# Performance work log

Hardware: AMD Instinct MI355X
Metric: run time of the kernel (lower is better)

## Reference

```python
import jax, jax.numpy as jnp
import numpy as np

N, D, H = 50000, 128, 2        # nodes, hidden_size(=ffn_size=out_channels), heads
E = 800000                      # edges
C = D                           # per-head out_channels (PyG TransformerConv)
EPS = 1e-5

def layer_norm(x, g, b):
    mu = jnp.mean(x, axis=-1, keepdims=True)
    var = jnp.mean((x - mu) ** 2, axis=-1, keepdims=True)
    return (x - mu) / jnp.sqrt(var + EPS) * g + b

def setup_inputs() -> dict:
    key = jax.random.key(0)
    ks = jax.random.split(key, 16)
    s_in = 1.0 / np.sqrt(D)
    s_ffn = 1.0 / np.sqrt(D)
    return {
        "x": jax.random.normal(ks[0], (N, D), jnp.float32),
        "edge_index": jax.random.randint(ks[1], (2, E), 0, N, jnp.int64),
        "ln1_g": jnp.ones((D,), jnp.float32),
        "ln1_b": jnp.zeros((D,), jnp.float32),
        "Wq": jax.random.normal(ks[2], (D, H * C), jnp.float32) * s_in,
        "bq": jnp.zeros((H * C,), jnp.float32),
        "Wk": jax.random.normal(ks[3], (D, H * C), jnp.float32) * s_in,
        "bk": jnp.zeros((H * C,), jnp.float32),
        "Wv": jax.random.normal(ks[4], (D, H * C), jnp.float32) * s_in,
        "bv": jnp.zeros((H * C,), jnp.float32),
        "Wskip": jax.random.normal(ks[5], (D, C), jnp.float32) * s_in,
        "bskip": jnp.zeros((C,), jnp.float32),
        "ln2_g": jnp.ones((D,), jnp.float32),
        "ln2_b": jnp.zeros((D,), jnp.float32),
        "W1": jax.random.normal(ks[6], (D, D), jnp.float32) * s_ffn,
        "b1": jnp.zeros((D,), jnp.float32),
        "W2": jax.random.normal(ks[7], (D, D), jnp.float32) * s_ffn,
        "b2": jnp.zeros((D,), jnp.float32),
    }

def reference(x, edge_index, ln1_g, ln1_b, Wq, bq, Wk, bk, Wv, bv,
              Wskip, bskip, ln2_g, ln2_b, W1, b1, W2, b2):
    src, dst = edge_index[0], edge_index[1]  # messages flow src(j) -> dst(i)
    n = x.shape[0]

    # --- self-attention block (pre-norm) ---
    y = layer_norm(x, ln1_g, ln1_b)
    q = (y @ Wq + bq).reshape(n, H, C)
    k = (y @ Wk + bk).reshape(n, H, C)
    v = (y @ Wv + bv).reshape(n, H, C)

    # per-edge attention logits [E, H]
    alpha = jnp.einsum('ehc,ehc->eh', q[dst], k[src]) / jnp.sqrt(jnp.float32(C))
    # softmax over incoming edges of each dst node
    m = jax.ops.segment_max(alpha, dst, num_segments=n)          # [N, H]
    p = jnp.exp(alpha - m[dst])                                  # [E, H]
    denom = jax.ops.segment_sum(p, dst, num_segments=n)          # [N, H]
    a = p / denom[dst]                                           # [E, H]

    attn = jax.ops.segment_sum(a[:, :, None] * v[src], dst, num_segments=n)  # [N,H,C]
    out = attn.mean(axis=1) + (y @ Wskip + bskip)  # concat=False mean + root skip
    x = x + out  # residual (dropout is identity at eval)

    # --- FFN block (pre-norm) ---
    h = layer_norm(x, ln2_g, ln2_b)
    h = jax.nn.gelu(h @ W1 + b1, approximate=False) @ W2 + b2
    return x + h
```

## Files before the change

kernel.cpp:

```cpp
#include <hip/hip_runtime.h>
#include <hip/hip_bf16.h>
#include <math.h>


typedef unsigned short u16;
using short8 = __attribute__((ext_vector_type(8))) short;
using f32x4  = __attribute__((ext_vector_type(4))) float;
using f32x2  = __attribute__((ext_vector_type(2))) float;

__device__ __forceinline__ float bf2f(u16 u) {
    return __uint_as_float(((unsigned int)u) << 16);
}
__device__ __forceinline__ u16 f2bf(float f) {
    __hip_bfloat16 h = __float2bfloat16(f);
    return __builtin_bit_cast(u16, h);
}
__device__ __forceinline__ float bfe(short8 v, int j) {
    return bf2f((u16)v[j]);
}
__device__ __forceinline__ void fp8x4_to_f32(int w, float* out) {
    f32x2 lo = __builtin_amdgcn_cvt_pk_f32_fp8(w, false);
    f32x2 hi = __builtin_amdgcn_cvt_pk_f32_fp8(w, true);
    out[0] = lo[0]; out[1] = lo[1]; out[2] = hi[0]; out[3] = hi[1];
}
__device__ __forceinline__ unsigned pack_fp8x4(float4 f) {
    unsigned w = 0;
    w = (unsigned)__builtin_amdgcn_cvt_pk_fp8_f32(f.x, f.y, (int)w, false);
    w = (unsigned)__builtin_amdgcn_cvt_pk_fp8_f32(f.z, f.w, (int)w, true);
    return w;
}

__global__ __launch_bounds__(256) void fused_prep_ln(
    const float* __restrict__ x, const float* __restrict__ ln1g,
    const float* __restrict__ ln1b,
    const float* __restrict__ Wq, const float* __restrict__ Wk,
    const float* __restrict__ Wv, const float* __restrict__ Ws,
    const float* __restrict__ W1, const float* __restrict__ W2,
    const float* __restrict__ bq, const float* __restrict__ bk,
    const float* __restrict__ bv, const float* __restrict__ bs,
    u16* __restrict__ wt, float* __restrict__ bc,
    u16* __restrict__ y, int* __restrict__ cnt, int n,
    const int* __restrict__ edst, int e, int histBlocks)
{
    if (blockIdx.x < (unsigned)histBlocks) {
        int stride = histBlocks * 256;
        for (int i = blockIdx.x * 256 + threadIdx.x; i < e; i += stride)
            atomicAdd(&cnt[edst[i]], 1);
        return;
    }
    int gsz = (gridDim.x - histBlocks) * 256;
    int gtid = (blockIdx.x - histBlocks) * 256 + threadIdx.x;

    for (int i = gtid; i < 147456 + 896; i += gsz) {
        if (i < 147456) {
            const float* W; int N; int base;
            if      (i <  32768) { W = Wq; N = 256; base = 0; }
            else if (i <  65536) { W = Wk; N = 256; base = 32768; }
            else if (i <  98304) { W = Wv; N = 256; base = 65536; }
            else if (i < 114688) { W = Ws; N = 128; base = 98304; }
            else if (i < 131072) { W = W1; N = 128; base = 114688; }
            else                 { W = W2; N = 128; base = 131072; }
            int j = i - base;
            int nIdx = j >> 7, k = j & 127;
            wt[i] = f2bf(W[(size_t)k * N + nIdx]);
        } else {
            int j = i - 147456;
            float v;
            if      (j < 256) v = bq[j];
            else if (j < 512) v = bk[j - 256];
            else if (j < 768) v = bv[j - 512];
            else              v = bs[j - 768];
            bc[j] = v;
        }
    }
    int lane = threadIdx.x & 63;
    int gw = gtid >> 6, nw = gsz >> 6;
    for (int row = gw; row < n; row += nw) {
        size_t base = (size_t)row * 128;
        float v0 = x[base + lane];
        float v1 = x[base + 64 + lane];
        float s1 = v0 + v1, s2 = v0 * v0 + v1 * v1;
        for (int o = 1; o <= 32; o <<= 1) {
            s1 += __shfl_xor(s1, o);
            s2 += __shfl_xor(s2, o);
        }
        float mu = s1 * (1.f / 128.f);
        float var = s2 * (1.f / 128.f) - mu * mu;
        float rstd = rsqrtf(var + 1e-5f);
        y[base + lane]      = f2bf((v0 - mu) * rstd * ln1g[lane] + ln1b[lane]);
        y[base + 64 + lane] = f2bf((v1 - mu) * rstd * ln1g[64 + lane] + ln1b[64 + lane]);
    }
}

__global__ __launch_bounds__(256) void scan_block_sum(const int* __restrict__ cnt,
                                                      int* __restrict__ bsum, int n) {
    __shared__ int s[256];
    int idx = blockIdx.x * 256 + threadIdx.x;
    s[threadIdx.x] = (idx < n) ? cnt[idx] : 0;
    __syncthreads();
    for (int o = 128; o > 0; o >>= 1) {
        if (threadIdx.x < o) s[threadIdx.x] += s[threadIdx.x + o];
        __syncthreads();
    }
    if (threadIdx.x == 0) bsum[blockIdx.x] = s[0];
}
__global__ __launch_bounds__(256) void scan_partials(const int* __restrict__ bsum,
                                                     int* __restrict__ bsumex, int nb) {
    __shared__ int s[256];
    int t = threadIdx.x;
    int v = (t < nb) ? bsum[t] : 0;
    s[t] = v;
    __syncthreads();
    for (int o = 1; o < 256; o <<= 1) {
        int add = (t >= o) ? s[t - o] : 0;
        __syncthreads();
        s[t] += add;
        __syncthreads();
    }
    bsumex[t] = s[t] - v;
}
__global__ __launch_bounds__(256) void scan_write(const int* __restrict__ cnt,
                                                  const int* __restrict__ bsumex,
                                                  int* __restrict__ rowptr,
                                                  int* __restrict__ cursor, int n, int etot) {
    __shared__ int s[256];
    int t = threadIdx.x;
    int idx = blockIdx.x * 256 + t;
    int v = (idx < n) ? cnt[idx] : 0;
    s[t] = v;
    __syncthreads();
    for (int o = 1; o < 256; o <<= 1) {
        int add = (t >= o) ? s[t - o] : 0;
        __syncthreads();
        s[t] += add;
        __syncthreads();
    }
    if (idx < n) {
        int ex = bsumex[blockIdx.x] + s[t] - v;
        rowptr[idx] = ex;
        cursor[idx] = ex;
    }
    if (idx == 0) rowptr[n] = etot;
}

__global__ __launch_bounds__(256, 6) void qkv_gemm(
    const u16* __restrict__ A, const u16* __restrict__ Bt,
    const float* __restrict__ bias, u16* __restrict__ qkv,
    float* __restrict__ skip, int n,
    const int* __restrict__ dst, const int* __restrict__ src,
    int* __restrict__ cursor, int* __restrict__ esrc, int e, int scatBlocks)
{
    __shared__ float epi[4][32 * 33];
    if (blockIdx.x < (unsigned)scatBlocks) {
        int stride = scatBlocks * 256;
        int i = blockIdx.x * 256 + threadIdx.x;
        for (; i + 3 * stride < e; i += 4 * stride) {
            int d0 = dst[i],              s0 = src[i];
            int d1 = dst[i + stride],     s1 = src[i + stride];
            int d2 = dst[i + 2 * stride], s2 = src[i + 2 * stride];
            int d3 = dst[i + 3 * stride], s3 = src[i + 3 * stride];
            int p0 = atomicAdd(&cursor[d0], 1);
            int p1 = atomicAdd(&cursor[d1], 1);
            int p2 = atomicAdd(&cursor[d2], 1);
            int p3 = atomicAdd(&cursor[d3], 1);
            esrc[p0] = s0; esrc[p1] = s1; esrc[p2] = s2; esrc[p3] = s3;
        }
        for (; i < e; i += stride) {
            int p = atomicAdd(&cursor[dst[i]], 1);
            esrc[p] = src[i];
        }
        return;
    }
    int bid = blockIdx.x - scatBlocks;
    int wc = threadIdx.x >> 6, lane = threadIdx.x & 63;
    int r0 = bid * 32;
    int lm = lane & 15, quad = lane >> 4;

    int ar0 = r0 + lm;       if (ar0 > n - 1) ar0 = n - 1;
    int ar1 = r0 + 16 + lm;  if (ar1 > n - 1) ar1 = n - 1;
    const u16* aB0 = A + (size_t)ar0 * 128 + quad * 8;
    const u16* aB1 = A + (size_t)ar1 * 128 + quad * 8;
    short8 a0_0 = *(const short8*)(aB0 + 0);
    short8 a0_1 = *(const short8*)(aB0 + 32);
    short8 a0_2 = *(const short8*)(aB0 + 64);
    short8 a0_3 = *(const short8*)(aB0 + 96);
    short8 a1_0 = *(const short8*)(aB1 + 0);
    short8 a1_1 = *(const short8*)(aB1 + 32);
    short8 a1_2 = *(const short8*)(aB1 + 64);
    short8 a1_3 = *(const short8*)(aB1 + 96);
    asm volatile("" : "+v"(a0_0), "+v"(a0_1), "+v"(a0_2), "+v"(a0_3),
                      "+v"(a1_0), "+v"(a1_1), "+v"(a1_2), "+v"(a1_3));

    int rr = lane & 31, hh = lane >> 5;
    int row = r0 + rr;
    bool rowOk = row < n;
    float* ep = epi[wc];

    for (int by = 0; by < 7; ++by) {
        int c0 = by * 128;
        const u16* bBase = Bt + (size_t)(c0 + wc * 32 + lm) * 128 + quad * 8;
        f32x4 acc[2][2] = {};
#pragma unroll
        for (int kx = 0; kx < 4; ++kx) {
            short8 a0 = (kx == 0) ? a0_0 : (kx == 1) ? a0_1 : (kx == 2) ? a0_2 : a0_3;
            short8 a1 = (kx == 0) ? a1_0 : (kx == 1) ? a1_1 : (kx == 2) ? a1_2 : a1_3;
#pragma unroll
            for (int j = 0; j < 2; ++j) {
                short8 bj = *(const short8*)(bBase + (size_t)j * 16 * 128 + kx * 32);
                acc[0][j] = __builtin_amdgcn_mfma_f32_16x16x32_bf16(a0, bj, acc[0][j], 0, 0, 0);
                acc[1][j] = __builtin_amdgcn_mfma_f32_16x16x32_bf16(a1, bj, acc[1][j], 0, 0, 0);
            }
        }
#pragma unroll
        for (int j = 0; j < 2; ++j) {
            float bv = bias[c0 + wc * 32 + j * 16 + lm];
#pragma unroll
            for (int rt = 0; rt < 2; ++rt)
#pragma unroll
                for (int i2 = 0; i2 < 4; ++i2)
                    ep[(rt * 16 + quad * 4 + i2) * 33 + j * 16 + lm]
                        = acc[rt][j][i2] + bv;
        }
        if (rowOk) {
            const float* ws = ep + rr * 33 + hh * 16;
            int colW = wc * 32 + hh * 16;
            if (c0 < 256) {
                u16* dp = qkv + (size_t)row * 640 + c0 + colW;
                short8 o0, o1;
#pragma unroll
                for (int jj = 0; jj < 8; ++jj) {
                    o0[jj] = (short)f2bf(ws[jj]);
                    o1[jj] = (short)f2bf(ws[8 + jj]);
                }
                *(short8*)(dp + 0) = o0;
                *(short8*)(dp + 8) = o1;
            } else if (c0 < 512) {
                unsigned char* kb = (unsigned char*)qkv + (size_t)row * 1280
                                    + 512 + (c0 - 256) + colW;
                uint4 o;
                o.x = pack_fp8x4(make_float4(ws[0],  ws[1],  ws[2],  ws[3]));
                o.y = pack_fp8x4(make_float4(ws[4],  ws[5],  ws[6],  ws[7]));
                o.z = pack_fp8x4(make_float4(ws[8],  ws[9],  ws[10], ws[11]));
                o.w = pack_fp8x4(make_float4(ws[12], ws[13], ws[14], ws[15]));
                *(uint4*)kb = o;
            } else if (c0 < 768) {
                u16* dp = qkv + (size_t)row * 640 + 384 + (c0 - 512) + colW;
                short8 o0, o1;
#pragma unroll
                for (int jj = 0; jj < 8; ++jj) {
                    o0[jj] = (short)f2bf(ws[jj]);
                    o1[jj] = (short)f2bf(ws[8 + jj]);
                }
                *(short8*)(dp + 0) = o0;
                *(short8*)(dp + 8) = o1;
            } else {
                float* dp = skip + (size_t)row * 128 + colW;
#pragma unroll
                for (int m2 = 0; m2 < 4; ++m2)
                    *(float4*)(dp + m2 * 4) = *(const float4*)(ws + m2 * 4);
            }
        }
    }
}

__global__ __launch_bounds__(256) void attn_kernel(
    const u16* __restrict__ qkv, const int* __restrict__ rowptr,
    const int* __restrict__ esrc, const float* __restrict__ x,
    float* __restrict__ sx, const float* __restrict__ g2,
    const float* __restrict__ b2, u16* __restrict__ y, int n)
{
    int wid = threadIdx.x >> 6, lane = threadIdx.x & 63;
    int i = blockIdx.x * 4 + wid;
    if (i >= n) return;
    int slot = lane >> 5;
    int sub  = lane & 15;
    int colOff = ((lane >> 4) & 1) * 128 + sub * 8;

    const float scale = 0.08838834764831845f;
    short8 q8 = *(const short8*)(qkv + (size_t)i * 640 + colOff);
    float qf[8];
#pragma unroll
    for (int j = 0; j < 8; ++j) qf[j] = bfe(q8, j) * scale;

    int beg = rowptr[i], end = rowptr[i + 1];
    float l = 0.f;
    float acc[8] = {};

    int t = beg + slot;
    for (; t + 6 < end; t += 8) {
        int s0 = esrc[t], s1 = esrc[t + 2], s2 = esrc[t + 4], s3 = esrc[t + 6];
        const u16* n0 = qkv + (size_t)s0 * 640;
        const u16* n1 = qkv + (size_t)s1 * 640;
        const u16* n2 = qkv + (size_t)s2 * 640;
        const u16* n3 = qkv + (size_t)s3 * 640;
        uint2 kw0 = *(const uint2*)((const unsigned char*)(n0 + 256) + colOff);
        uint2 kw1 = *(const uint2*)((const unsigned char*)(n1 + 256) + colOff);
        uint2 kw2 = *(const uint2*)((const unsigned char*)(n2 + 256) + colOff);
        uint2 kw3 = *(const uint2*)((const unsigned char*)(n3 + 256) + colOff);
        short8 v0 = *(const short8*)(n0 + 384 + colOff);
        short8 v1 = *(const short8*)(n1 + 384 + colOff);
        short8 v2 = *(const short8*)(n2 + 384 + colOff);
        short8 v3 = *(const short8*)(n3 + 384 + colOff);
        float k0f[8], k1f[8], k2f[8], k3f[8];
        fp8x4_to_f32((int)kw0.x, k0f); fp8x4_to_f32((int)kw0.y, k0f + 4);
        fp8x4_to_f32((int)kw1.x, k1f); fp8x4_to_f32((int)kw1.y, k1f + 4);
        fp8x4_to_f32((int)kw2.x, k2f); fp8x4_to_f32((int)kw2.y, k2f + 4);
        fp8x4_to_f32((int)kw3.x, k3f); fp8x4_to_f32((int)kw3.y, k3f + 4);
        float d0 = 0.f, d1 = 0.f, d2 = 0.f, d3 = 0.f;
#pragma unroll
        for (int j = 0; j < 8; ++j) {
            d0 += qf[j] * k0f[j];
            d1 += qf[j] * k1f[j];
            d2 += qf[j] * k2f[j];
            d3 += qf[j] * k3f[j];
        }
#pragma unroll
        for (int o = 1; o <= 8; o <<= 1) {
            d0 += __shfl_xor(d0, o);
            d1 += __shfl_xor(d1, o);
            d2 += __shfl_xor(d2, o);
            d3 += __shfl_xor(d3, o);
        }
        float w0 = __expf(d0), w1 = __expf(d1);
        float w2 = __expf(d2), w3 = __expf(d3);
        l += w0 + w1 + w2 + w3;
#pragma unroll
        for (int j = 0; j < 8; ++j)
            acc[j] += w0 * bfe(v0, j) + w1 * bfe(v1, j)
                    + w2 * bfe(v2, j) + w3 * bfe(v3, j);
    }
    for (; t < end; t += 2) {
        int s0 = esrc[t];
        const u16* n0 = qkv + (size_t)s0 * 640;
        uint2 kw0 = *(const uint2*)((const unsigned char*)(n0 + 256) + colOff);
        short8 v0 = *(const short8*)(n0 + 384 + colOff);
        float k0f[8];
        fp8x4_to_f32((int)kw0.x, k0f); fp8x4_to_f32((int)kw0.y, k0f + 4);
        float d0 = 0.f;
#pragma unroll
        for (int j = 0; j < 8; ++j) d0 += qf[j] * k0f[j];
#pragma unroll
        for (int o = 1; o <= 8; o <<= 1) d0 += __shfl_xor(d0, o);
        float w0 = __expf(d0);
        l += w0;
#pragma unroll
        for (int j = 0; j < 8; ++j) acc[j] += w0 * bfe(v0, j);
    }

    l += __shfl_xor(l, 32);
    float inv = (l > 0.f) ? (1.f / l) : 0.f;
#pragma unroll
    for (int j = 0; j < 8; ++j) {
        acc[j] = (acc[j] + __shfl_xor(acc[j], 32)) * inv;
        acc[j] = 0.5f * (acc[j] + __shfl_xor(acc[j], 16));
    }

    if (lane < 16) {
        size_t base = (size_t)i * 128 + sub * 8;
        float4 xv0 = *(const float4*)(x + base);
        float4 xv1 = *(const float4*)(x + base + 4);
        float4 sk0 = *(const float4*)(sx + base);
        float4 sk1 = *(const float4*)(sx + base + 4);
        float r[8];
        r[0] = xv0.x + sk0.x + acc[0]; r[1] = xv0.y + sk0.y + acc[1];
        r[2] = xv0.z + sk0.z + acc[2]; r[3] = xv0.w + sk0.w + acc[3];
        r[4] = xv1.x + sk1.x + acc[4]; r[5] = xv1.y + sk1.y + acc[5];
        r[6] = xv1.z + sk1.z + acc[6]; r[7] = xv1.w + sk1.w + acc[7];
        *(float4*)(sx + base)     = make_float4(r[0], r[1], r[2], r[3]);
        *(float4*)(sx + base + 4) = make_float4(r[4], r[5], r[6], r[7]);
        float s1 = 0.f, s2 = 0.f;
#pragma unroll
        for (int j = 0; j < 8; ++j) { s1 += r[j]; s2 += r[j] * r[j]; }
#pragma unroll
        for (int o = 1; o <= 8; o <<= 1) {
            s1 += __shfl_xor(s1, o);
            s2 += __shfl_xor(s2, o);
        }
        float mu = s1 * (1.f / 128.f);
        float var = s2 * (1.f / 128.f) - mu * mu;
        float rstd = rsqrtf(var + 1e-5f);
        short8 o8;
#pragma unroll
        for (int j = 0; j < 8; ++j)
            o8[j] = (short)f2bf((r[j] - mu) * rstd * g2[sub * 8 + j] + b2[sub * 8 + j]);
        *(short8*)(y + base) = o8;
    }
}

__global__ __launch_bounds__(256) void ffn_kernel(
    const u16* __restrict__ y2, const u16* __restrict__ W1T,
    const float* __restrict__ b1, const u16* __restrict__ W2T,
    const float* __restrict__ b2, const float* __restrict__ x2,
    float* __restrict__ out, int n)
{
    __shared__ u16 t1[64 * 136];
    int wid = threadIdx.x >> 6, lane = threadIdx.x & 63;
    int lm = lane & 15, quad = lane >> 4;
    int r0 = blockIdx.x * 64 + wid * 16;

    const u16* aBase = y2 + (size_t)(r0 + lm) * 128 + quad * 8;
    f32x4 acc[8] = {};
#pragma unroll
    for (int kk = 0; kk < 128; kk += 32) {
        short8 a0 = *(const short8*)(aBase + kk);
#pragma unroll
        for (int j = 0; j < 8; ++j) {
            short8 bj = *(const short8*)(W1T + (size_t)(j * 16 + lm) * 128 + quad * 8 + kk);
            acc[j] = __builtin_amdgcn_mfma_f32_16x16x32_bf16(a0, bj, acc[j], 0, 0, 0);
        }
    }
#pragma unroll
    for (int j = 0; j < 8; ++j) {
        int col = j * 16 + lm;
        float bv = b1[col];
#pragma unroll
        for (int i2 = 0; i2 < 4; ++i2) {
            int rl = wid * 16 + quad * 4 + i2;
            float v = acc[j][i2] + bv;
            v = 0.5f * v * (1.f + erff(v * 0.70710678118654752f));
            t1[rl * 136 + col] = f2bf(v);
        }
    }
    __syncthreads();

    f32x4 acc2[8] = {};
#pragma unroll
    for (int kk = 0; kk < 128; kk += 32) {
        short8 a0 = *(const short8*)(t1 + (wid * 16 + lm) * 136 + quad * 8 + kk);
#pragma unroll
        for (int j = 0; j < 8; ++j) {
            short8 bj = *(const short8*)(W2T + (size_t)(j * 16 + lm) * 128 + quad * 8 + kk);
            acc2[j] = __builtin_amdgcn_mfma_f32_16x16x32_bf16(a0, bj, acc2[j], 0, 0, 0);
        }
    }
#pragma unroll
    for (int j = 0; j < 8; ++j) {
        int col = j * 16 + lm;
        float bv = b2[col];
#pragma unroll
        for (int i2 = 0; i2 < 4; ++i2) {
            int row = r0 + quad * 4 + i2;
            if (row >= n) continue;
            size_t ob = (size_t)row * 128 + col;
            out[ob] = acc2[j][i2] + bv + x2[ob];
        }
    }
}

extern "C" void kernel_launch(void* const* d_in, const int* in_sizes, int n_in,
                              void* d_out, int out_size, void* d_ws, size_t ws_size,
                              hipStream_t stream)
{
    const float* x    = (const float*)d_in[0];
    const int*   ei   = (const int*)d_in[1];

    int n = in_sizes[0] / 128;
    int e = in_sizes[1] / 2;
    const int* src  = ei;
    const int* dstp = ei + e;

    char* w = (char*)d_ws;
    size_t off = 0;
    auto alloc = [&](size_t bytes) -> void* {
        void* p = w + off;
        off = (off + bytes + 255) & ~(size_t)255;
        return p;
    };
    u16*   y    = (u16*)alloc((size_t)n * 128 * 2);
    u16*   qkv  = (u16*)alloc((size_t)n * 640 * 2);
    float* sx   = (float*)alloc((size_t)n * 128 * 4);
    u16*   wt   = (u16*)alloc((size_t)147456 * 2);
    float* bc   = (float*)alloc(896 * 4);
    int* cnt    = (int*)alloc((size_t)n * 4);
    int* cursor = (int*)alloc((size_t)n * 4);
    int* rowptr = (int*)alloc(((size_t)n + 1) * 4);
    int* esrc   = (int*)alloc((size_t)e * 4);
    int* bsum   = (int*)alloc(1024);
    int* bsumex = (int*)alloc(1024);

    int gr   = (n + 63) / 64;
    int gr32 = (n + 31) / 32;
    int nb   = (n + 255) / 256;
    int scatBlocks = 512;
    int histBlocks = 512;

    hipMemsetAsync(cnt, 0, (size_t)n * sizeof(int), stream);
    fused_prep_ln<<<2048 + histBlocks, 256, 0, stream>>>(
        x, (const float*)d_in[2], (const float*)d_in[3],
        (const float*)d_in[4], (const float*)d_in[6], (const float*)d_in[8],
        (const float*)d_in[10], (const float*)d_in[14], (const float*)d_in[16],
        (const float*)d_in[5], (const float*)d_in[7], (const float*)d_in[9],
        (const float*)d_in[11], wt, bc, y, cnt, n, dstp, e, histBlocks);
    scan_block_sum<<<nb, 256, 0, stream>>>(cnt, bsum, n);
    scan_partials<<<1, 256, 0, stream>>>(bsum, bsumex, nb);
    scan_write<<<nb, 256, 0, stream>>>(cnt, bsumex, rowptr, cursor, n, e);
    qkv_gemm<<<scatBlocks + gr32, 256, 0, stream>>>(
        y, wt, bc, qkv, sx, n, dstp, src, cursor, esrc, e, scatBlocks);
    attn_kernel<<<(n + 3) / 4, 256, 0, stream>>>(qkv, rowptr, esrc, x, sx,
                                                 (const float*)d_in[12],
                                                 (const float*)d_in[13], y, n);
    ffn_kernel<<<gr, 256, 0, stream>>>(y, wt + 114688, (const float*)d_in[15],
                                       wt + 131072, (const float*)d_in[17],
                                       sx, (float*)d_out, n);
}
```

Measured before the change: 405.2 us.

## Record per-edge rank during histogram to replace scatter atomics in CSR build

The histogram pass now stores the value returned by each atomicAdd as that edge's rank within its destination bucket. The scatter pass then computes each edge's CSR slot as rowptr[dst] + rank with plain loads, so the second round of contended atomics and the cursor array are no longer needed. This costs an extra E-sized int array written and read back, and the number of scatter blocks is doubled. Edge order within each destination changes, which can slightly perturb the floating-point summation order.

```diff
diff --git a/kernel.cpp b/kernel.cpp
--- a/kernel.cpp
+++ b/kernel.cpp
@@ -39,13 +39,13 @@
     const float* __restrict__ bq, const float* __restrict__ bk,
     const float* __restrict__ bv, const float* __restrict__ bs,
     u16* __restrict__ wt, float* __restrict__ bc,
-    u16* __restrict__ y, int* __restrict__ cnt, int n,
+    u16* __restrict__ y, int* __restrict__ cnt, int* __restrict__ rank, int n,
     const int* __restrict__ edst, int e, int histBlocks)
 {
     if (blockIdx.x < (unsigned)histBlocks) {
         int stride = histBlocks * 256;
         for (int i = blockIdx.x * 256 + threadIdx.x; i < e; i += stride)
-            atomicAdd(&cnt[edst[i]], 1);
+            rank[i] = atomicAdd(&cnt[edst[i]], 1);
         return;
     }
     int gsz = (gridDim.x - histBlocks) * 256;
@@ -122,7 +122,7 @@
 __global__ __launch_bounds__(256) void scan_write(const int* __restrict__ cnt,
                                                   const int* __restrict__ bsumex,
                                                   int* __restrict__ rowptr,
-                                                  int* __restrict__ cursor, int n, int etot) {
+                                                  int n, int etot) {
     __shared__ int s[256];
     int t = threadIdx.x;
     int idx = blockIdx.x * 256 + t;
@@ -135,11 +135,7 @@
         s[t] += add;
         __syncthreads();
     }
-    if (idx < n) {
-        int ex = bsumex[blockIdx.x] + s[t] - v;
-        rowptr[idx] = ex;
-        cursor[idx] = ex;
-    }
+    if (idx < n) rowptr[idx] = bsumex[blockIdx.x] + s[t] - v;
     if (idx == 0) rowptr[n] = etot;
 }
 
@@ -148,27 +144,24 @@
     const float* __restrict__ bias, u16* __restrict__ qkv,
     float* __restrict__ skip, int n,
     const int* __restrict__ dst, const int* __restrict__ src,
-    int* __restrict__ cursor, int* __restrict__ esrc, int e, int scatBlocks)
+    const int* __restrict__ rank, const int* __restrict__ rowptr,
+    int* __restrict__ esrc, int e, int scatBlocks)
 {
     __shared__ float epi[4][32 * 33];
     if (blockIdx.x < (unsigned)scatBlocks) {
         int stride = scatBlocks * 256;
         int i = blockIdx.x * 256 + threadIdx.x;
         for (; i + 3 * stride < e; i += 4 * stride) {
-            int d0 = dst[i],              s0 = src[i];
-            int d1 = dst[i + stride],     s1 = src[i + stride];
-            int d2 = dst[i + 2 * stride], s2 = src[i + 2 * stride];
-            int d3 = dst[i + 3 * stride], s3 = src[i + 3 * stride];
-            int p0 = atomicAdd(&cursor[d0], 1);
-            int p1 = atomicAdd(&cursor[d1], 1);
-            int p2 = atomicAdd(&cursor[d2], 1);
-            int p3 = atomicAdd(&cursor[d3], 1);
-            esrc[p0] = s0; esrc[p1] = s1; esrc[p2] = s2; esrc[p3] = s3;
-        }
-        for (; i < e; i += stride) {
-            int p = atomicAdd(&cursor[dst[i]], 1);
-            esrc[p] = src[i];
-        }
+            int i1 = i + stride, i2 = i + 2 * stride, i3 = i + 3 * stride;
+            int d0 = dst[i],  d1 = dst[i1], d2 = dst[i2], d3 = dst[i3];
+            int r0 = rank[i], r1 = rank[i1], r2 = rank[i2], r3 = rank[i3];
+            int s0 = src[i],  s1 = src[i1], s2 = src[i2], s3 = src[i3];
+            int p0 = rowptr[d0], p1 = rowptr[d1], p2 = rowptr[d2], p3 = rowptr[d3];
+            esrc[p0 + r0] = s0; esrc[p1 + r1] = s1;
+            esrc[p2 + r2] = s2; esrc[p3 + r3] = s3;
+        }
+        for (; i < e; i += stride)
+            esrc[rowptr[dst[i]] + rank[i]] = src[i];
         return;
     }
     int bid = blockIdx.x - scatBlocks;
@@ -472,7 +465,7 @@
     u16*   wt   = (u16*)alloc((size_t)147456 * 2);
     float* bc   = (float*)alloc(896 * 4);
     int* cnt    = (int*)alloc((size_t)n * 4);
-    int* cursor = (int*)alloc((size_t)n * 4);
+    int* rankA  = (int*)alloc((size_t)e * 4);
     int* rowptr = (int*)alloc(((size_t)n + 1) * 4);
     int* esrc   = (int*)alloc((size_t)e * 4);
     int* bsum   = (int*)alloc(1024);
@@ -481,7 +474,7 @@
     int gr   = (n + 63) / 64;
     int gr32 = (n + 31) / 32;
     int nb   = (n + 255) / 256;
-    int scatBlocks = 512;
+    int scatBlocks = 1024;
     int histBlocks = 512;
 
     hipMemsetAsync(cnt, 0, (size_t)n * sizeof(int), stream);
@@ -490,12 +483,12 @@
         (const float*)d_in[4], (const float*)d_in[6], (const float*)d_in[8],
         (const float*)d_in[10], (const float*)d_in[14], (const float*)d_in[16],
         (const float*)d_in[5], (const float*)d_in[7], (const float*)d_in[9],
-        (const float*)d_in[11], wt, bc, y, cnt, n, dstp, e, histBlocks);
+        (const float*)d_in[11], wt, bc, y, cnt, rankA, n, dstp, e, histBlocks);
     scan_block_sum<<<nb, 256, 0, stream>>>(cnt, bsum, n);
     scan_partials<<<1, 256, 0, stream>>>(bsum, bsumex, nb);
-    scan_write<<<nb, 256, 0, stream>>>(cnt, bsumex, rowptr, cursor, n, e);
+    scan_write<<<nb, 256, 0, stream>>>(cnt, bsumex, rowptr, n, e);
     qkv_gemm<<<scatBlocks + gr32, 256, 0, stream>>>(
-        y, wt, bc, qkv, sx, n, dstp, src, cursor, esrc, e, scatBlocks);
+        y, wt, bc, qkv, sx, n, dstp, src, rankA, rowptr, esrc, e, scatBlocks);
     attn_kernel<<<(n + 3) / 4, 256, 0, stream>>>(qkv, rowptr, esrc, x, sx,
                                                  (const float*)d_in[12],
                                                  (const float*)d_in[13], y, n);
```

New measurement: 369.8 us. 8.7% less time.
